# Optimization experiments

Hardware: AMD Instinct MI355X
Metric: run time of the kernel (lower is better)

## Reference

```python
import jax, jax.numpy as jnp
import numpy as np

BITS = 16          # number of histogram bins == number of spiking time steps
B, IN_DIM, HID = 16384, 784, 128


def setup_inputs() -> dict:
    key = jax.random.key(0)
    ks = jax.random.split(key, 9)
    dims = [(HID, IN_DIM), (HID, HID), (HID, HID), (IN_DIM, HID)]
    inp = {"features": jax.random.uniform(ks[0], (B, IN_DIM), jnp.float32)}
    for i, (o, d) in enumerate(dims):
        inp["W%d" % i] = jax.random.normal(ks[1 + i], (o, d), jnp.float32) * 0.05
        inp["b%d" % i] = jax.random.normal(ks[5 + i], (o,), jnp.float32) * 0.05
    # np.histogram_bin_edges(bins=16) -> 17 uniformly spaced edges per layer
    in_max = [1.0, 4.0, 4.0, 4.0]
    out_max = [4.0, 4.0, 4.0, 4.0]
    for i in range(4):
        inp["in_bins%d" % i] = jnp.linspace(0.0, in_max[i], BITS + 1, dtype=jnp.float32)
        inp["out_bins%d" % i] = jnp.linspace(0.0, out_max[i], BITS + 1, dtype=jnp.float32)
    return inp


def _spike(t):
    # output[output>1]=1; output[output<1]=0  (==1 stays 1)  -> (t >= 1)
    # totals[output==1] -= 1
    s = (t >= 1.0).astype(t.dtype)
    return s, t - s


def _forward(features, Ws, bs, in_bins, out_bins):
    h_in = [e[1] - e[0] for e in in_bins]    # uniform spike heights
    h_out = [e[1] - e[0] for e in out_bins]
    # set_up_weights: weight *= h_in; weight /= h_out (bias likewise)
    Weff = [Ws[l] * (h_in[l] / h_out[l]) for l in range(4)]
    beff = [bs[l] * (h_in[l] / h_out[l]) for l in range(4)]
    n = features.shape[0]
    # discretize: np.digitize(x, in_bins) - 1, then / 16.0 (non-differentiable)
    act = (jnp.digitize(jax.lax.stop_gradient(features), in_bins[0]) - 1).astype(features.dtype) / BITS
    t_in = jnp.zeros_like(features)                               # input-layer membrane
    totals = tuple(jnp.broadcast_to(beff[l], (n,) + beff[l].shape) for l in range(4))  # reset_totals: totals = bias
    out_acc = jnp.zeros((n, Weff[3].shape[0]), features.dtype)

    def step(carry, _):
        t_in, t0, t1, t2, t3, out = carry
        s_in, t_in = _spike(t_in + act)
        # process_layer: totals += sum(weight * spikes, axis=1) == spikes @ W.T
        s0, t0 = _spike(t0 + s_in @ Weff[0].T)
        s1, t1 = _spike(t1 + s0 @ Weff[1].T)
        s2, t2 = _spike(t2 + s1 @ Weff[2].T)
        s3, t3 = _spike(t3 + s2 @ Weff[3].T)
        return (t_in, t0, t1, t2, t3, out + s3), None

    carry, _ = jax.lax.scan(step, (t_in,) + totals + (out_acc,), None, length=BITS)
    out_spikes = carry[-1]
    # decoder_output_layer.reconstruct: spikes * (out_bins[1] - out_bins[0])
    return out_spikes * h_out[3]


def reference(features, W0, W1, W2, W3, b0, b1, b2, b3,
              in_bins0, in_bins1, in_bins2, in_bins3,
              out_bins0, out_bins1, out_bins2, out_bins3):
    return _forward(features,
                    [W0, W1, W2, W3], [b0, b1, b2, b3],
                    [in_bins0, in_bins1, in_bins2, in_bins3],
                    [out_bins0, out_bins1, out_bins2, out_bins3])
```

## Files before the change

kernel.cpp:

```cpp
#include <hip/hip_runtime.h>

#define IN_DIM 784
#define HID 128
#define NSTEP 16
#define BATCH 16384

typedef float v2f __attribute__((ext_vector_type(2)));
typedef float v4f __attribute__((ext_vector_type(4)));
typedef unsigned long long ull;

constexpr int W0T_OFF = 0;
constexpr int W1T_OFF = W0T_OFF + IN_DIM*HID;
constexpr int W2T_OFF = W1T_OFF + HID*HID;
constexpr int W3T_OFF = W2T_OFF + HID*HID;
constexpr int B0_OFF  = W3T_OFF + HID*IN_DIM;
constexpr int B1_OFF  = B0_OFF + HID;
constexpr int B2_OFF  = B1_OFF + HID;
constexpr int B3_OFF  = B2_OFF + HID;
constexpr int WS_FLOATS = B3_OFF + IN_DIM;
constexpr int MASK_OFF  = WS_FLOATS;

constexpr int CHUNK_COLS = 32;
constexpr int CHUNK_F    = CHUNK_COLS * HID;
constexpr int NCHUNK     = 25;

constexpr int TPB   = 512;
constexpr int WAVES = TPB / 64;

__global__ __launch_bounds__(256) void prep_kernel(
    const float* __restrict__ W0, const float* __restrict__ b0,
    const float* __restrict__ W1, const float* __restrict__ b1,
    const float* __restrict__ W2, const float* __restrict__ b2,
    const float* __restrict__ W3, const float* __restrict__ b3,
    const float* __restrict__ ib0, const float* __restrict__ ob0,
    const float* __restrict__ ib1, const float* __restrict__ ob1,
    const float* __restrict__ ib2, const float* __restrict__ ob2,
    const float* __restrict__ ib3, const float* __restrict__ ob3,
    float* __restrict__ ws)
{
    int idx = blockIdx.x * 256 + threadIdx.x;
    if (idx >= WS_FLOATS) return;
    float r0 = (ib0[1] - ib0[0]) / (ob0[1] - ob0[0]);
    float r1 = (ib1[1] - ib1[0]) / (ob1[1] - ob1[0]);
    float r2 = (ib2[1] - ib2[0]) / (ob2[1] - ob2[0]);
    float r3 = (ib3[1] - ib3[0]) / (ob3[1] - ob3[0]);
    if (idx < W1T_OFF) {
        int t = idx;            int k = t >> 7, j = t & 127;
        ws[idx] = W0[j * IN_DIM + k] * r0;
    } else if (idx < W2T_OFF) {
        int t = idx - W1T_OFF;  int k = t >> 7, j = t & 127;
        ws[idx] = W1[j * HID + k] * r1;
    } else if (idx < W3T_OFF) {
        int t = idx - W2T_OFF;  int k = t >> 7, j = t & 127;
        ws[idx] = W2[j * HID + k] * r2;
    } else if (idx < B0_OFF) {
        int t = idx - W3T_OFF;  int k = t / IN_DIM, o = t % IN_DIM;
        ws[idx] = W3[o * HID + k] * r3;
    } else if (idx < B1_OFF) ws[idx] = b0[idx - B0_OFF] * r0;
    else if (idx < B2_OFF)   ws[idx] = b1[idx - B1_OFF] * r1;
    else if (idx < B3_OFF)   ws[idx] = b2[idx - B2_OFF] * r2;
    else                     ws[idx] = b3[idx - B3_OFF] * r3;
}

__global__ __launch_bounds__(TPB) void snn_build(
    const float* __restrict__ feat,
    const float* __restrict__ ws,
    const float* __restrict__ ib0,
    ull* __restrict__ masks)
{
    __shared__ float smem[2 * CHUNK_F];

    const int tid  = threadIdx.x;
    const int lane = tid & 63;
    const int wid  = tid >> 6;
    const int sample = blockIdx.x * WAVES + wid;

    const float* W0t = ws + W0T_OFF;
    const float* frow = feat + (size_t)sample * IN_DIM;

    float edge[16];
#pragma unroll
    for (int e = 0; e < 16; ++e) edge[e] = ib0[e + 1];

    {
        const float4* g4 = (const float4*)W0t;
        float4* lb = (float4*)smem;
#pragma unroll
        for (int i = 0; i < 2; ++i) lb[i * TPB + tid] = g4[i * TPB + tid];
    }
    __syncthreads();

    v2f C[16];
#pragma unroll
    for (int mv = 0; mv < 16; ++mv) C[mv] = (v2f)(0.f);

    for (int c = 0; c < NCHUNK; ++c) {
        float4 rg0, rg1;
        {
            const float4* g4 = (const float4*)W0t + (size_t)(c + 1) * (CHUNK_F / 4);
            rg0 = g4[0 * TPB + tid];
            rg1 = g4[1 * TPB + tid];
        }

        int col = c * CHUNK_COLS + (lane & 31);
        bool valid = col < IN_DIM;
        float x = frow[valid ? col : 0];
        int mm = 0;
#pragma unroll
        for (int e = 0; e < 16; ++e) mm += (x >= edge[e]) ? 1 : 0;
        if (!valid) mm = -1;

        const v2f* bufp = (const v2f*)(smem + (c & 1) * CHUNK_F);
#pragma unroll
        for (int mv = 1; mv <= 16; ++mv) {
            unsigned mk = (unsigned)__ballot(mm == mv);
            v2f ca = (v2f)(0.f), cb = (v2f)(0.f);
            while (mk) {
                int b0 = __builtin_ctz(mk); mk &= mk - 1;
                v2f w0 = bufp[b0 * 64 + lane];
                if (mk) {
                    int b1 = __builtin_ctz(mk); mk &= mk - 1;
                    v2f w1 = bufp[b1 * 64 + lane];
                    if (mk) {
                        int b2 = __builtin_ctz(mk); mk &= mk - 1;
                        v2f w2 = bufp[b2 * 64 + lane];
                        if (mk) {
                            int b3i = __builtin_ctz(mk); mk &= mk - 1;
                            v2f w3 = bufp[b3i * 64 + lane];
                            cb += w3;
                        }
                        ca += w2;
                    }
                    cb += w1;
                }
                ca += w0;
            }
            C[mv - 1] += ca + cb;
        }

        if (c + 1 < NCHUNK) {
            float4* lb = (float4*)(smem + ((c + 1) & 1) * CHUNK_F);
            lb[0 * TPB + tid] = rg0;
            lb[1 * TPB + tid] = rg1;
        }
        __syncthreads();
    }

    v2f t0 = ((const v2f*)(ws + B0_OFF))[lane];
    ull* mrow = masks + (size_t)sample * 32;

    for (int s = 1; s <= NSTEP; ++s) {
#pragma unroll
        for (int mv = 1; mv <= 16; ++mv) {
            if (((s * mv) & 15) < mv) t0 += C[mv - 1];
        }
        bool px = (t0.x >= 1.0f), py = (t0.y >= 1.0f);
        ull mx = __ballot(px);
        ull my = __ballot(py);
        if (px) t0.x -= 1.0f;
        if (py) t0.y -= 1.0f;
        if (lane == 0) {
            mrow[2 * (s - 1)]     = mx;
            mrow[2 * (s - 1) + 1] = my;
        }
    }
}

__global__ __launch_bounds__(256) void snn_prop(
    const float* __restrict__ ws,
    const ull* __restrict__ masks,
    const float* __restrict__ ob3,
    float* __restrict__ out)
{
    const int tid  = threadIdx.x;
    const int lane = tid & 63;
    const int wid  = tid >> 6;
    const int sample = blockIdx.x * 4 + wid;

    const float* W1t = ws + W1T_OFF;
    const float* W2t = ws + W2T_OFF;
    const float* W3t = ws + W3T_OFF;
    const ull* mrow = masks + (size_t)sample * 32;

    v2f t1 = ((const v2f*)(ws + B1_OFF))[lane];
    v2f t2 = ((const v2f*)(ws + B2_OFF))[lane];
    v4f t3[4], cnt[4];
    {
        const v4f* b3v = (const v4f*)(ws + B3_OFF);
#pragma unroll
        for (int r = 0; r < 3; ++r) t3[r] = b3v[r * 64 + lane];
        t3[3] = (v4f)(0.f);
        if (lane < 4) t3[3] = b3v[192 + lane];
#pragma unroll
        for (int r = 0; r < 4; ++r) cnt[r] = (v4f)(0.f);
    }

    for (int s = 0; s < NSTEP; ++s) {
        ull vx = mrow[2 * s], vy = mrow[2 * s + 1];
        ull mx = ((ull)__builtin_amdgcn_readfirstlane((unsigned)(vx >> 32)) << 32)
               | __builtin_amdgcn_readfirstlane((unsigned)vx);
        ull my = ((ull)__builtin_amdgcn_readfirstlane((unsigned)(vy >> 32)) << 32)
               | __builtin_amdgcn_readfirstlane((unsigned)vy);

        {
            v2f ca = (v2f)(0.f), cb = (v2f)(0.f);
            while (mx) {
                int b0 = __builtin_ctzll(mx); mx &= mx - 1;
                v2f w0 = ((const v2f*)(W1t + (2 * b0) * HID))[lane];
                if (mx) {
                    int b1 = __builtin_ctzll(mx); mx &= mx - 1;
                    v2f w1 = ((const v2f*)(W1t + (2 * b1) * HID))[lane];
                    if (mx) {
                        int b2 = __builtin_ctzll(mx); mx &= mx - 1;
                        v2f w2 = ((const v2f*)(W1t + (2 * b2) * HID))[lane];
                        if (mx) {
                            int b3i = __builtin_ctzll(mx); mx &= mx - 1;
                            v2f w3 = ((const v2f*)(W1t + (2 * b3i) * HID))[lane];
                            cb += w3;
                        }
                        ca += w2;
                    }
                    cb += w1;
                }
                ca += w0;
            }
            while (my) {
                int b0 = __builtin_ctzll(my); my &= my - 1;
                v2f w0 = ((const v2f*)(W1t + (2 * b0 + 1) * HID))[lane];
                if (my) {
                    int b1 = __builtin_ctzll(my); my &= my - 1;
                    v2f w1 = ((const v2f*)(W1t + (2 * b1 + 1) * HID))[lane];
                    if (my) {
                        int b2 = __builtin_ctzll(my); my &= my - 1;
                        v2f w2 = ((const v2f*)(W1t + (2 * b2 + 1) * HID))[lane];
                        if (my) {
                            int b3i = __builtin_ctzll(my); my &= my - 1;
                            v2f w3 = ((const v2f*)(W1t + (2 * b3i + 1) * HID))[lane];
                            cb += w3;
                        }
                        ca += w2;
                    }
                    cb += w1;
                }
                ca += w0;
            }
            t1 += ca + cb;
        }
        {
            bool px = (t1.x >= 1.0f), py = (t1.y >= 1.0f);
            ull nx = __ballot(px);
            ull ny = __ballot(py);
            if (px) t1.x -= 1.0f;
            if (py) t1.y -= 1.0f;
            v2f ca = (v2f)(0.f), cb = (v2f)(0.f);
            while (nx) {
                int b0 = __builtin_ctzll(nx); nx &= nx - 1;
                v2f w0 = ((const v2f*)(W2t + (2 * b0) * HID))[lane];
                if (nx) {
                    int b1 = __builtin_ctzll(nx); nx &= nx - 1;
                    v2f w1 = ((const v2f*)(W2t + (2 * b1) * HID))[lane];
                    if (nx) {
                        int b2 = __builtin_ctzll(nx); nx &= nx - 1;
                        v2f w2 = ((const v2f*)(W2t + (2 * b2) * HID))[lane];
                        if (nx) {
                            int b3i = __builtin_ctzll(nx); nx &= nx - 1;
                            v2f w3 = ((const v2f*)(W2t + (2 * b3i) * HID))[lane];
                            cb += w3;
                        }
                        ca += w2;
                    }
                    cb += w1;
                }
                ca += w0;
            }
            while (ny) {
                int b0 = __builtin_ctzll(ny); ny &= ny - 1;
                v2f w0 = ((const v2f*)(W2t + (2 * b0 + 1) * HID))[lane];
                if (ny) {
                    int b1 = __builtin_ctzll(ny); ny &= ny - 1;
                    v2f w1 = ((const v2f*)(W2t + (2 * b1 + 1) * HID))[lane];
                    if (ny) {
                        int b2 = __builtin_ctzll(ny); ny &= ny - 1;
                        v2f w2 = ((const v2f*)(W2t + (2 * b2 + 1) * HID))[lane];
                        if (ny) {
                            int b3i = __builtin_ctzll(ny); ny &= ny - 1;
                            v2f w3 = ((const v2f*)(W2t + (2 * b3i + 1) * HID))[lane];
                            cb += w3;
                        }
                        ca += w2;
                    }
                    cb += w1;
                }
                ca += w0;
            }
            t2 += ca + cb;
        }
        {
            bool px = (t2.x >= 1.0f), py = (t2.y >= 1.0f);
            ull nx = __ballot(px);
            ull ny = __ballot(py);
            if (px) t2.x -= 1.0f;
            if (py) t2.y -= 1.0f;
            while (nx) {
                int b0 = __builtin_ctzll(nx); nx &= nx - 1;
                const v4f* c0 = (const v4f*)(W3t + (2 * b0) * IN_DIM);
                v4f x0 = c0[lane], x1 = c0[64 + lane], x2 = c0[128 + lane];
                v4f x3 = c0[192 + (lane & 3)];
                if (nx) {
                    int b1 = __builtin_ctzll(nx); nx &= nx - 1;
                    const v4f* c1 = (const v4f*)(W3t + (2 * b1) * IN_DIM);
                    v4f y0 = c1[lane], y1 = c1[64 + lane], y2 = c1[128 + lane];
                    v4f y3 = c1[192 + (lane & 3)];
                    t3[0] += y0; t3[1] += y1; t3[2] += y2;
                    if (lane < 4) t3[3] += y3;
                }
                t3[0] += x0; t3[1] += x1; t3[2] += x2;
                if (lane < 4) t3[3] += x3;
            }
            while (ny) {
                int b0 = __builtin_ctzll(ny); ny &= ny - 1;
                const v4f* c0 = (const v4f*)(W3t + (2 * b0 + 1) * IN_DIM);
                v4f x0 = c0[lane], x1 = c0[64 + lane], x2 = c0[128 + lane];
                v4f x3 = c0[192 + (lane & 3)];
                if (ny) {
                    int b1 = __builtin_ctzll(ny); ny &= ny - 1;
                    const v4f* c1 = (const v4f*)(W3t + (2 * b1 + 1) * IN_DIM);
                    v4f y0 = c1[lane], y1 = c1[64 + lane], y2 = c1[128 + lane];
                    v4f y3 = c1[192 + (lane & 3)];
                    t3[0] += y0; t3[1] += y1; t3[2] += y2;
                    if (lane < 4) t3[3] += y3;
                }
                t3[0] += x0; t3[1] += x1; t3[2] += x2;
                if (lane < 4) t3[3] += x3;
            }
        }
#pragma unroll
        for (int r = 0; r < 4; ++r) {
            if (t3[r].x >= 1.0f) { t3[r].x -= 1.0f; cnt[r].x += 1.0f; }
            if (t3[r].y >= 1.0f) { t3[r].y -= 1.0f; cnt[r].y += 1.0f; }
            if (t3[r].z >= 1.0f) { t3[r].z -= 1.0f; cnt[r].z += 1.0f; }
            if (t3[r].w >= 1.0f) { t3[r].w -= 1.0f; cnt[r].w += 1.0f; }
        }
    }

    const float h = ob3[1] - ob3[0];
    v4f* orow = (v4f*)(out + (size_t)sample * IN_DIM);
#pragma unroll
    for (int r = 0; r < 3; ++r)
        orow[r * 64 + lane] = cnt[r] * h;
    if (lane < 4)
        orow[192 + lane] = cnt[3] * h;
}

extern "C" void kernel_launch(void* const* d_in, const int* in_sizes, int n_in,
                              void* d_out, int out_size, void* d_ws, size_t ws_size,
                              hipStream_t stream)
{
    const float* feat = (const float*)d_in[0];
    const float* W0  = (const float*)d_in[1];
    const float* b0  = (const float*)d_in[2];
    const float* W1  = (const float*)d_in[3];
    const float* b1  = (const float*)d_in[4];
    const float* W2  = (const float*)d_in[5];
    const float* b2  = (const float*)d_in[6];
    const float* W3  = (const float*)d_in[7];
    const float* b3  = (const float*)d_in[8];
    const float* ib0 = (const float*)d_in[9];
    const float* ob0 = (const float*)d_in[10];
    const float* ib1 = (const float*)d_in[11];
    const float* ob1 = (const float*)d_in[12];
    const float* ib2 = (const float*)d_in[13];
    const float* ob2 = (const float*)d_in[14];
    const float* ib3 = (const float*)d_in[15];
    const float* ob3 = (const float*)d_in[16];
    float* ws  = (float*)d_ws;
    float* op  = (float*)d_out;
    ull* masks = (ull*)(ws + MASK_OFF);

    prep_kernel<<<(WS_FLOATS + 255) / 256, 256, 0, stream>>>(
        W0, b0, W1, b1, W2, b2, W3, b3,
        ib0, ob0, ib1, ob1, ib2, ob2, ib3, ob3, ws);

    snn_build<<<BATCH / WAVES, TPB, 0, stream>>>(feat, ws, ib0, masks);
    snn_prop<<<BATCH / 4, 256, 0, stream>>>(ws, masks, ob3, op);
}
```

Before: 435.5 us.

## Split wave into half-waves gathering float4 weight rows with padded LDS layout

Lays out the first-layer weight chunk in LDS as float4 rows with a padded stride of 33, and splits each wave into two 32-lane halves. Each half handles a different active input column and reads float4 (four hidden units) per lane, so each gather step covers two columns with wider loads. Partial sums are merged across the halves with a shuffle. Spike masks are rebuilt by interleaving the ballots through bit spreading so they keep the previous per-lane ordering. The intent is fewer, wider LDS reads per active column and fewer bank conflicts, at the cost of more registers for the float4 accumulators and some extra shuffle and bit-manipulation work.

```diff
diff --git a/kernel.cpp b/kernel.cpp
--- a/kernel.cpp
+++ b/kernel.cpp
@@ -21,11 +21,22 @@
 constexpr int MASK_OFF  = WS_FLOATS;
 
 constexpr int CHUNK_COLS = 32;
-constexpr int CHUNK_F    = CHUNK_COLS * HID;
+constexpr int COL_STRIDE = 132;
+constexpr int CHUNK_F    = 33 * COL_STRIDE;
 constexpr int NCHUNK     = 25;
 
 constexpr int TPB   = 512;
 constexpr int WAVES = TPB / 64;
+
+__device__ __forceinline__ ull spread32(unsigned v) {
+    ull x = v;
+    x = (x | (x << 16)) & 0x0000FFFF0000FFFFull;
+    x = (x | (x << 8))  & 0x00FF00FF00FF00FFull;
+    x = (x | (x << 4))  & 0x0F0F0F0F0F0F0F0Full;
+    x = (x | (x << 2))  & 0x3333333333333333ull;
+    x = (x | (x << 1))  & 0x5555555555555555ull;
+    return x;
+}
 
 __global__ __launch_bounds__(256) void prep_kernel(
     const float* __restrict__ W0, const float* __restrict__ b0,
@@ -72,6 +83,7 @@
 
     const int tid  = threadIdx.x;
     const int lane = tid & 63;
+    const int q    = lane & 31;
     const int wid  = tid >> 6;
     const int sample = blockIdx.x * WAVES + wid;
 
@@ -82,27 +94,33 @@
 #pragma unroll
     for (int e = 0; e < 16; ++e) edge[e] = ib0[e + 1];
 
+    if (tid < 32) {
+        float4 z = make_float4(0.f, 0.f, 0.f, 0.f);
+        ((float4*)smem)[32 * 33 + tid] = z;
+        ((float4*)(smem + CHUNK_F))[32 * 33 + tid] = z;
+    }
     {
         const float4* g4 = (const float4*)W0t;
         float4* lb = (float4*)smem;
-#pragma unroll
-        for (int i = 0; i < 2; ++i) lb[i * TPB + tid] = g4[i * TPB + tid];
+        float4 a = g4[tid], b = g4[512 + tid];
+        lb[(tid >> 5) * 33 + (tid & 31)] = a;
+        lb[(16 + (tid >> 5)) * 33 + (tid & 31)] = b;
     }
     __syncthreads();
 
-    v2f C[16];
-#pragma unroll
-    for (int mv = 0; mv < 16; ++mv) C[mv] = (v2f)(0.f);
+    v4f C[16];
+#pragma unroll
+    for (int mv = 0; mv < 16; ++mv) C[mv] = (v4f)(0.f);
 
     for (int c = 0; c < NCHUNK; ++c) {
         float4 rg0, rg1;
         {
-            const float4* g4 = (const float4*)W0t + (size_t)(c + 1) * (CHUNK_F / 4);
-            rg0 = g4[0 * TPB + tid];
-            rg1 = g4[1 * TPB + tid];
-        }
-
-        int col = c * CHUNK_COLS + (lane & 31);
+            const float4* g4 = (const float4*)W0t + (size_t)(c + 1) * 1024;
+            rg0 = g4[tid];
+            rg1 = g4[512 + tid];
+        }
+
+        int col = c * CHUNK_COLS + q;
         bool valid = col < IN_DIM;
         float x = frow[valid ? col : 0];
         int mm = 0;
@@ -110,27 +128,21 @@
         for (int e = 0; e < 16; ++e) mm += (x >= edge[e]) ? 1 : 0;
         if (!valid) mm = -1;
 
-        const v2f* bufp = (const v2f*)(smem + (c & 1) * CHUNK_F);
+        const v4f* bufp = (const v4f*)(smem + (c & 1) * CHUNK_F);
 #pragma unroll
         for (int mv = 1; mv <= 16; ++mv) {
             unsigned mk = (unsigned)__ballot(mm == mv);
-            v2f ca = (v2f)(0.f), cb = (v2f)(0.f);
+            v4f ca = (v4f)(0.f), cb = (v4f)(0.f);
             while (mk) {
                 int b0 = __builtin_ctz(mk); mk &= mk - 1;
-                v2f w0 = bufp[b0 * 64 + lane];
+                int b1 = mk ? __builtin_ctz(mk) : 32; mk &= mk - 1;
+                int cA = (lane < 32) ? b0 : b1;
+                v4f w0 = bufp[cA * 33 + q];
                 if (mk) {
-                    int b1 = __builtin_ctz(mk); mk &= mk - 1;
-                    v2f w1 = bufp[b1 * 64 + lane];
-                    if (mk) {
-                        int b2 = __builtin_ctz(mk); mk &= mk - 1;
-                        v2f w2 = bufp[b2 * 64 + lane];
-                        if (mk) {
-                            int b3i = __builtin_ctz(mk); mk &= mk - 1;
-                            v2f w3 = bufp[b3i * 64 + lane];
-                            cb += w3;
-                        }
-                        ca += w2;
-                    }
+                    int b2 = __builtin_ctz(mk); mk &= mk - 1;
+                    int b3 = mk ? __builtin_ctz(mk) : 32; mk &= mk - 1;
+                    int cB = (lane < 32) ? b2 : b3;
+                    v4f w1 = bufp[cB * 33 + q];
                     cb += w1;
                 }
                 ca += w0;
@@ -140,13 +152,23 @@
 
         if (c + 1 < NCHUNK) {
             float4* lb = (float4*)(smem + ((c + 1) & 1) * CHUNK_F);
-            lb[0 * TPB + tid] = rg0;
-            lb[1 * TPB + tid] = rg1;
+            lb[(tid >> 5) * 33 + (tid & 31)] = rg0;
+            lb[(16 + (tid >> 5)) * 33 + (tid & 31)] = rg1;
         }
         __syncthreads();
     }
 
-    v2f t0 = ((const v2f*)(ws + B0_OFF))[lane];
+#pragma unroll
+    for (int mv = 0; mv < 16; ++mv) {
+        v4f o;
+        o.x = __shfl_xor(C[mv].x, 32);
+        o.y = __shfl_xor(C[mv].y, 32);
+        o.z = __shfl_xor(C[mv].z, 32);
+        o.w = __shfl_xor(C[mv].w, 32);
+        C[mv] += o;
+    }
+
+    v4f t0 = ((const v4f*)(ws + B0_OFF))[q];
     ull* mrow = masks + (size_t)sample * 32;
 
     for (int s = 1; s <= NSTEP; ++s) {
@@ -154,11 +176,16 @@
         for (int mv = 1; mv <= 16; ++mv) {
             if (((s * mv) & 15) < mv) t0 += C[mv - 1];
         }
-        bool px = (t0.x >= 1.0f), py = (t0.y >= 1.0f);
-        ull mx = __ballot(px);
-        ull my = __ballot(py);
-        if (px) t0.x -= 1.0f;
-        if (py) t0.y -= 1.0f;
+        unsigned m0 = (unsigned)__ballot(t0.x >= 1.0f);
+        unsigned m1 = (unsigned)__ballot(t0.y >= 1.0f);
+        unsigned m2 = (unsigned)__ballot(t0.z >= 1.0f);
+        unsigned m3 = (unsigned)__ballot(t0.w >= 1.0f);
+        if (t0.x >= 1.0f) t0.x -= 1.0f;
+        if (t0.y >= 1.0f) t0.y -= 1.0f;
+        if (t0.z >= 1.0f) t0.z -= 1.0f;
+        if (t0.w >= 1.0f) t0.w -= 1.0f;
+        ull mx = spread32(m0) | (spread32(m2) << 1);
+        ull my = spread32(m1) | (spread32(m3) << 1);
         if (lane == 0) {
             mrow[2 * (s - 1)]     = mx;
             mrow[2 * (s - 1) + 1] = my;
```

After: 746.9 us. 71.5% more time.
